# Optimization experiments

Hardware: AMD Instinct MI355X
Metric: run time of the kernel (lower is better)

The kernel has to match this reference:

```python
import jax, jax.numpy as jnp
import numpy as np

N, C, HH, WW = 16, 512, 64, 96
FEAT_STRIDE = 16
RATIOS = (0.5, 1.0, 2.0)
SCALES = (8.0, 16.0, 32.0)
BASE = 16.0
NA = len(RATIOS) * len(SCALES)  # 9 anchors per location


def _anchor_base():
    py = px = BASE / 2.0
    rows = []
    for r in RATIOS:
        for s in SCALES:
            h = BASE * s * np.sqrt(r)
            w = BASE * s * np.sqrt(1.0 / r)
            rows.append([py - h / 2.0, px - w / 2.0, py + h / 2.0, px + w / 2.0])
    return np.asarray(rows, dtype=np.float32)


def _shifted_anchors(hh, ww):
    # mirrors enumerate_shifted_anchor body (which lacks a return in the source)
    ab = _anchor_base()
    y = np.arange(hh, dtype=np.float32) * FEAT_STRIDE
    x = np.arange(ww, dtype=np.float32) * FEAT_STRIDE
    mx, my = np.meshgrid(x, y)
    shift = np.stack([my.ravel(), mx.ravel(), my.ravel(), mx.ravel()], axis=1)
    return (shift[:, None, :] + ab[None, :, :]).reshape(-1, 4).astype(np.float32)


def setup_inputs() -> dict:
    key = jax.random.key(0)
    ks = jax.random.split(key, 3)
    x = jax.random.normal(ks[0], (N, C, HH, WW), dtype=jnp.float32)
    # small init scale keeps softmax unsaturated (512-dim contraction)
    loc_w = jax.random.normal(ks[1], (NA * 4, C), dtype=jnp.float32) * 0.01
    loc_b = jnp.zeros((NA * 4,), dtype=jnp.float32)
    score_w = jax.random.normal(ks[2], (NA * 2, C), dtype=jnp.float32) * 0.01
    score_b = jnp.zeros((NA * 2,), dtype=jnp.float32)
    return {"x": x, "loc_w": loc_w, "loc_b": loc_b, "score_w": score_w, "score_b": score_b}


def reference(x, loc_w, loc_b, score_w, score_b):
    n, _, hh, ww = x.shape
    anchor = jnp.asarray(_shifted_anchors(hh, ww))  # (hh*ww*NA, 4)
    # NOTE: source computes h = relu(conv1(x)) but then applies loc/score to x
    # (h is dead code), so the faithful reference applies the 1x1 convs to x.
    # 1x1 conv == channel contraction; permute(0,2,3,1) folded into einsum output order.
    rpn_loc = jnp.einsum('nchw,oc->nhwo', x, loc_w) + loc_b          # (n, hh, ww, 36)
    rpn_loc = rpn_loc.reshape(n, -1, 4)                               # (n, hh*ww*NA, 4)
    rpn_score = jnp.einsum('nchw,oc->nhwo', x, score_w) + score_b    # (n, hh, ww, 18)
    sm = jax.nn.softmax(rpn_score.reshape(n, hh, ww, NA, 2), axis=-1)
    rpn_fg_scores = sm[..., 1].reshape(n, -1)                         # (n, hh*ww*NA)
    return rpn_loc, rpn_score, rpn_fg_scores, anchor
```

## Files before the change

### kernel.cpp

```cpp
#include <hip/hip_runtime.h>
#include <hip/hip_bf16.h>
#include <math.h>

#define CC 512
#define HH 64
#define WW 96
#define NN 16
#define HW (HH*WW)
#define NA 9
#define NLOC 36
#define NSC 18
#define NO_PAD 64

typedef __attribute__((ext_vector_type(4))) float f32x4;
typedef __attribute__((ext_vector_type(8))) short s16x8;

__device__ __forceinline__ unsigned short f2bf(float f) {
    __hip_bfloat16 h = __float2bfloat16(f);
    union { __hip_bfloat16 h; unsigned short u; } cv;
    cv.h = h;
    return cv.u;
}
__device__ __forceinline__ unsigned pk2(float lo, float hi) {
    return (unsigned)f2bf(lo) | ((unsigned)f2bf(hi) << 16);
}

__global__ void prep_kernel(const float* __restrict__ lw,
                            const float* __restrict__ sw,
                            unsigned short* __restrict__ wbf,
                            float* __restrict__ out3) {
    int b = blockIdx.x;
    if (b < 128) {
        int i = b * 256 + threadIdx.x;
        int o = i >> 9, c = i & 511;
        float v = 0.0f;
        if (o < NLOC) v = lw[o * CC + c];
        else if (o < 54) v = sw[(o - NLOC) * CC + c];
        wbf[i] = f2bf(v);
    } else {
        int t = (b - 128) * 256 + threadIdx.x;
        if (t >= HW * NA) return;
        int a   = t % NA;
        int rem = t / NA;
        int h = rem / WW, w = rem % WW;
        int ri = a / 3, si = a % 3;
        const double ratios[3] = {0.5, 1.0, 2.0};
        const double scales[3] = {8.0, 16.0, 32.0};
        double ha = 16.0 * scales[si] * sqrt(ratios[ri]);
        double wa = 16.0 * scales[si] * sqrt(1.0 / ratios[ri]);
        float y1 = (float)(8.0 - ha * 0.5);
        float x1 = (float)(8.0 - wa * 0.5);
        float y2 = (float)(8.0 + ha * 0.5);
        float x2 = (float)(8.0 + wa * 0.5);
        float sy = (float)(h * 16);
        float sx = (float)(w * 16);
        float4 v = make_float4(sy + y1, sx + x1, sy + y2, sx + x2);
        *reinterpret_cast<float4*>(out3 + (size_t)t * 4) = v;
    }
}

__launch_bounds__(256, 3)
__global__ void rpn_mfma_kernel(const float* __restrict__ x,
                                const unsigned short* __restrict__ wbf,
                                const float* __restrict__ lb,
                                const float* __restrict__ sb,
                                float* __restrict__ out0,
                                float* __restrict__ out1,
                                float* __restrict__ out2) {
    const int tid  = threadIdx.x;
    const int lane = tid & 63;
    const int w    = tid >> 6;
    const int col  = lane & 15;
    const int rgrp = lane >> 4;
    const int krow = rgrp * 8;

    const int bid  = blockIdx.x;
    const int swz  = (bid & 7) * 96 + (bid >> 3);
    const int pbase = swz * 128;
    const int n     = pbase / HW;
    const int rem   = pbase % HW;
    const float* xA0 = x + (size_t)n * CC * HW + rem + w * 16 + col;
    const float* xA1 = xA0 + 64;

    f32x4 acc0[4], acc1[4];
    #pragma unroll
    for (int nt = 0; nt < 4; ++nt) {
        acc0[nt] = (f32x4){0.f, 0.f, 0.f, 0.f};
        acc1[nt] = (f32x4){0.f, 0.f, 0.f, 0.f};
    }

    float a0[8], a1[8], p0[8], p1[8];
    #pragma unroll
    for (int j = 0; j < 8; ++j) {
        a0[j] = xA0[(size_t)(krow + j) * HW];
        a1[j] = xA1[(size_t)(krow + j) * HW];
    }

    #pragma unroll 2
    for (int ks = 0; ks < 16; ++ks) {
        const int kb = ks * 32;
        if (ks < 15) {
            #pragma unroll
            for (int j = 0; j < 8; ++j) {
                p0[j] = xA0[(size_t)(kb + 32 + krow + j) * HW];
                p1[j] = xA1[(size_t)(kb + 32 + krow + j) * HW];
            }
        }
        s16x8 bfr[4];
        #pragma unroll
        for (int nt = 0; nt < 4; ++nt)
            bfr[nt] = *reinterpret_cast<const s16x8*>(
                wbf + (size_t)(nt * 16 + col) * CC + kb + krow);
        union { unsigned u[4]; s16x8 v; } fa0, fa1;
        #pragma unroll
        for (int j = 0; j < 4; ++j) {
            fa0.u[j] = pk2(a0[2 * j], a0[2 * j + 1]);
            fa1.u[j] = pk2(a1[2 * j], a1[2 * j + 1]);
        }

        #pragma unroll
        for (int nt = 0; nt < 4; ++nt)
            acc0[nt] = __builtin_amdgcn_mfma_f32_16x16x32_bf16(fa0.v, bfr[nt], acc0[nt], 0, 0, 0);
        #pragma unroll
        for (int nt = 0; nt < 4; ++nt)
            acc1[nt] = __builtin_amdgcn_mfma_f32_16x16x32_bf16(fa1.v, bfr[nt], acc1[nt], 0, 0, 0);

        #pragma unroll
        for (int j = 0; j < 8; ++j) { a0[j] = p0[j]; a1[j] = p1[j]; }
    }

    #pragma unroll
    for (int m = 0; m < 2; ++m) {
        #pragma unroll
        for (int nt = 0; nt < 4; ++nt) {
            int o = nt * 16 + col;
            float bias = (o < NLOC) ? lb[o] : ((o < 54) ? sb[o - NLOC] : 0.0f);
            #pragma unroll
            for (int r = 0; r < 4; ++r) {
                float val  = (m == 0 ? acc0[nt][r] : acc1[nt][r]) + bias;
                float part = __shfl_xor(val, 1);
                int p = pbase + w * 16 + m * 64 + rgrp * 4 + r;
                if (o < NLOC) {
                    out0[(size_t)p * NLOC + o] = val;
                } else if (o < 54) {
                    int os = o - NLOC;
                    out1[(size_t)p * NSC + os] = val;
                    if ((os & 1) == 0)
                        out2[(size_t)p * NA + (os >> 1)] = 1.0f / (1.0f + __expf(val - part));
                }
            }
        }
    }
}

extern "C" void kernel_launch(void* const* d_in, const int* in_sizes, int n_in,
                              void* d_out, int out_size, void* d_ws, size_t ws_size,
                              hipStream_t stream) {
    const float* x  = (const float*)d_in[0];
    const float* lw = (const float*)d_in[1];
    const float* lb = (const float*)d_in[2];
    const float* sw = (const float*)d_in[3];
    const float* sb = (const float*)d_in[4];

    float* out0 = (float*)d_out;
    float* out1 = out0 + (size_t)NN * HW * NLOC;
    float* out2 = out1 + (size_t)NN * HW * NSC;
    float* out3 = out2 + (size_t)NN * HW * NA;

    unsigned short* wbf = (unsigned short*)d_ws;

    prep_kernel<<<344, 256, 0, stream>>>(lw, sw, wbf, out3);

    int grid_m = NN * HW / 128;
    rpn_mfma_kernel<<<grid_m, 256, 0, stream>>>(x, wbf, lb, sb, out0, out1, out2);
}
```

Baseline: 51.94 us.

## Vectorize x loads as float2 pairs and fuse anchor generation into GEMM kernel

Each lane now loads two adjacent pixels with one 8-byte load instead of two scalar loads 64 pixels apart, and the two MFMA row tiles become interleaved even/odd pixels, with output indexing remapped to match. Anchor generation moves from the prep kernel into the tail of the main kernel (72 anchors per block), so the prep kernel only converts weights. This is meant to cut load instruction count and shrink the prep launch. In exchange the main kernel does extra double-precision work per block, and the output stores become less contiguous.

```diff
diff --git a/kernel.cpp b/kernel.cpp
--- a/kernel.cpp
+++ b/kernel.cpp
@@ -13,6 +13,7 @@
 #define NO_PAD 64
 
 typedef __attribute__((ext_vector_type(4))) float f32x4;
+typedef __attribute__((ext_vector_type(2))) float f32x2;
 typedef __attribute__((ext_vector_type(8))) short s16x8;
 
 __device__ __forceinline__ unsigned short f2bf(float f) {
@@ -25,38 +26,16 @@
     return (unsigned)f2bf(lo) | ((unsigned)f2bf(hi) << 16);
 }
 
-__global__ void prep_kernel(const float* __restrict__ lw,
-                            const float* __restrict__ sw,
-                            unsigned short* __restrict__ wbf,
-                            float* __restrict__ out3) {
-    int b = blockIdx.x;
-    if (b < 128) {
-        int i = b * 256 + threadIdx.x;
-        int o = i >> 9, c = i & 511;
-        float v = 0.0f;
-        if (o < NLOC) v = lw[o * CC + c];
-        else if (o < 54) v = sw[(o - NLOC) * CC + c];
-        wbf[i] = f2bf(v);
-    } else {
-        int t = (b - 128) * 256 + threadIdx.x;
-        if (t >= HW * NA) return;
-        int a   = t % NA;
-        int rem = t / NA;
-        int h = rem / WW, w = rem % WW;
-        int ri = a / 3, si = a % 3;
-        const double ratios[3] = {0.5, 1.0, 2.0};
-        const double scales[3] = {8.0, 16.0, 32.0};
-        double ha = 16.0 * scales[si] * sqrt(ratios[ri]);
-        double wa = 16.0 * scales[si] * sqrt(1.0 / ratios[ri]);
-        float y1 = (float)(8.0 - ha * 0.5);
-        float x1 = (float)(8.0 - wa * 0.5);
-        float y2 = (float)(8.0 + ha * 0.5);
-        float x2 = (float)(8.0 + wa * 0.5);
-        float sy = (float)(h * 16);
-        float sx = (float)(w * 16);
-        float4 v = make_float4(sy + y1, sx + x1, sy + y2, sx + x2);
-        *reinterpret_cast<float4*>(out3 + (size_t)t * 4) = v;
-    }
+__global__ void prep_w_kernel(const float* __restrict__ lw,
+                              const float* __restrict__ sw,
+                              unsigned short* __restrict__ wbf) {
+    int i = blockIdx.x * 256 + threadIdx.x;
+    if (i >= NO_PAD * CC) return;
+    int o = i >> 9, c = i & 511;
+    float v = 0.0f;
+    if (o < NLOC) v = lw[o * CC + c];
+    else if (o < 54) v = sw[(o - NLOC) * CC + c];
+    wbf[i] = f2bf(v);
 }
 
 __launch_bounds__(256, 3)
@@ -66,7 +45,8 @@
                                 const float* __restrict__ sb,
                                 float* __restrict__ out0,
                                 float* __restrict__ out1,
-                                float* __restrict__ out2) {
+                                float* __restrict__ out2,
+                                float* __restrict__ out3) {
     const int tid  = threadIdx.x;
     const int lane = tid & 63;
     const int w    = tid >> 6;
@@ -79,8 +59,7 @@
     const int pbase = swz * 128;
     const int n     = pbase / HW;
     const int rem   = pbase % HW;
-    const float* xA0 = x + (size_t)n * CC * HW + rem + w * 16 + col;
-    const float* xA1 = xA0 + 64;
+    const float* xA = x + (size_t)n * CC * HW + rem + w * 32 + 2 * col;
 
     f32x4 acc0[4], acc1[4];
     #pragma unroll
@@ -89,22 +68,19 @@
         acc1[nt] = (f32x4){0.f, 0.f, 0.f, 0.f};
     }
 
-    float a0[8], a1[8], p0[8], p1[8];
+    f32x2 a[8], p[8];
     #pragma unroll
-    for (int j = 0; j < 8; ++j) {
-        a0[j] = xA0[(size_t)(krow + j) * HW];
-        a1[j] = xA1[(size_t)(krow + j) * HW];
-    }
+    for (int j = 0; j < 8; ++j)
+        a[j] = *reinterpret_cast<const f32x2*>(xA + (size_t)(krow + j) * HW);
 
     #pragma unroll 2
     for (int ks = 0; ks < 16; ++ks) {
         const int kb = ks * 32;
         if (ks < 15) {
             #pragma unroll
-            for (int j = 0; j < 8; ++j) {
-                p0[j] = xA0[(size_t)(kb + 32 + krow + j) * HW];
-                p1[j] = xA1[(size_t)(kb + 32 + krow + j) * HW];
-            }
+            for (int j = 0; j < 8; ++j)
+                p[j] = *reinterpret_cast<const f32x2*>(
+                    xA + (size_t)(kb + 32 + krow + j) * HW);
         }
         s16x8 bfr[4];
         #pragma unroll
@@ -114,8 +90,8 @@
         union { unsigned u[4]; s16x8 v; } fa0, fa1;
         #pragma unroll
         for (int j = 0; j < 4; ++j) {
-            fa0.u[j] = pk2(a0[2 * j], a0[2 * j + 1]);
-            fa1.u[j] = pk2(a1[2 * j], a1[2 * j + 1]);
+            fa0.u[j] = pk2(a[2 * j].x, a[2 * j + 1].x);
+            fa1.u[j] = pk2(a[2 * j].y, a[2 * j + 1].y);
         }
 
         #pragma unroll
@@ -126,7 +102,7 @@
             acc1[nt] = __builtin_amdgcn_mfma_f32_16x16x32_bf16(fa1.v, bfr[nt], acc1[nt], 0, 0, 0);
 
         #pragma unroll
-        for (int j = 0; j < 8; ++j) { a0[j] = p0[j]; a1[j] = p1[j]; }
+        for (int j = 0; j < 8; ++j) a[j] = p[j];
     }
 
     #pragma unroll
@@ -139,17 +115,37 @@
             for (int r = 0; r < 4; ++r) {
                 float val  = (m == 0 ? acc0[nt][r] : acc1[nt][r]) + bias;
                 float part = __shfl_xor(val, 1);
-                int p = pbase + w * 16 + m * 64 + rgrp * 4 + r;
+                int pgl = pbase + w * 32 + 2 * (rgrp * 4 + r) + m;
                 if (o < NLOC) {
-                    out0[(size_t)p * NLOC + o] = val;
+                    out0[(size_t)pgl * NLOC + o] = val;
                 } else if (o < 54) {
                     int os = o - NLOC;
-                    out1[(size_t)p * NSC + os] = val;
+                    out1[(size_t)pgl * NSC + os] = val;
                     if ((os & 1) == 0)
-                        out2[(size_t)p * NA + (os >> 1)] = 1.0f / (1.0f + __expf(val - part));
+                        out2[(size_t)pgl * NA + (os >> 1)] = 1.0f / (1.0f + __expf(val - part));
                 }
             }
         }
+    }
+
+    if (tid < 72) {
+        int t = bid * 72 + tid;
+        int a9   = t % NA;
+        int rem2 = t / NA;
+        int h = rem2 / WW, ww2 = rem2 % WW;
+        int ri = a9 / 3, si = a9 % 3;
+        const double ratios[3] = {0.5, 1.0, 2.0};
+        const double scales[3] = {8.0, 16.0, 32.0};
+        double ha = 16.0 * scales[si] * sqrt(ratios[ri]);
+        double wa = 16.0 * scales[si] * sqrt(1.0 / ratios[ri]);
+        float y1 = (float)(8.0 - ha * 0.5);
+        float x1 = (float)(8.0 - wa * 0.5);
+        float y2 = (float)(8.0 + ha * 0.5);
+        float x2 = (float)(8.0 + wa * 0.5);
+        float sy = (float)(h * 16);
+        float sx = (float)(ww2 * 16);
+        float4 v = make_float4(sy + y1, sx + x1, sy + y2, sx + x2);
+        *reinterpret_cast<float4*>(out3 + (size_t)t * 4) = v;
     }
 }
 
@@ -169,8 +165,9 @@
 
     unsigned short* wbf = (unsigned short*)d_ws;
 
-    prep_kernel<<<344, 256, 0, stream>>>(lw, sw, wbf, out3);
+    int grid_w = (NO_PAD * CC + 255) / 256;
+    prep_w_kernel<<<grid_w, 256, 0, stream>>>(lw, sw, wbf);
 
     int grid_m = NN * HW / 128;
-    rpn_mfma_kernel<<<grid_m, 256, 0, stream>>>(x, wbf, lb, sb, out0, out1, out2);
+    rpn_mfma_kernel<<<grid_m, 256, 0, stream>>>(x, wbf, lb, sb, out0, out1, out2, out3);
 }
```

Result: no change. 51.83 us (-0.2%).
